# Performance work log

Measured on AMD Instinct MI355X. Metric: run time of the kernel, lower is better.

## Reference

```python
import jax, jax.numpy as jnp
import numpy as np

B, D, K = 8192, 128, 256
RHO = 1.0


def setup_inputs() -> dict:
    key = jax.random.key(0)
    k1, k2, k3 = jax.random.split(key, 3)
    h = jax.random.normal(k1, (B, D), dtype=jnp.float32)
    y = jax.random.randint(k2, (B,), 0, K, dtype=jnp.int64)
    centers = jax.random.normal(k3, (K, D), dtype=jnp.float32)  # nn.Parameter
    return {"h": h, "y": y, "centers": centers}


def reference(h, y, centers):
    # Pairwise squared distances h[b] vs centers[k]: (B, K)
    diff = h[:, None, :] - centers[None, :, :]          # (B, K, D) broadcast
    norm_sq = jnp.sum(diff * diff, axis=2)              # (B, K)
    # Gather distance to the true-class centroid
    distance = jnp.take_along_axis(norm_sq, y[:, None], axis=1)[:, 0]  # (B,)
    # logsumexp over negative euclidean distances
    logsum = jax.nn.logsumexp(-jnp.sqrt(norm_sq), axis=1)              # (B,)
    loss = jnp.mean(distance + logsum)                  # reduction='mean'
    # Regularization: repel nearest centroids (num_classes != 1)
    cdiff = centers[:, None, :] - centers[None, :, :]   # (K, K, D)
    pd = jnp.sum(cdiff * cdiff, axis=2)                 # squared cdist (K, K)
    pd = jnp.where(jnp.eye(K, dtype=bool), jnp.inf, pd)
    reg = jnp.sum(-jnp.min(jnp.log(pd), axis=-1))       # reduction='sum'
    return loss + RHO * reg
```

## Files before the change

kernel.cpp:

```cpp
#include <hip/hip_runtime.h>
#include <math.h>

typedef __attribute__((ext_vector_type(8))) __bf16 bf16x8;
typedef __attribute__((ext_vector_type(4))) float f32x4;

constexpr int B = 8192;
constexpr int D = 128;
constexpr int K = 256;
constexpr int MB = B / 16;


__global__ __launch_bounds__(256) void prep_kernel(const float* __restrict__ centers,
                                                   float* __restrict__ part_reg,
                                                   float* __restrict__ cc,
                                                   bf16x8* __restrict__ cbu) {
  __shared__ float red[4];
  const int lane = threadIdx.x & 63;
  const int wid  = threadIdx.x >> 6;
  if (blockIdx.x < K) {
    const int i = blockIdx.x;
    const int j = threadIdx.x;
    const float* ci = centers + (size_t)i * D;
    const float* cj = centers + (size_t)j * D;
    float pd = 0.f;
#pragma unroll
    for (int q = 0; q < D / 4; ++q) {
      float4 a  = reinterpret_cast<const float4*>(ci)[q];
      float4 bq = reinterpret_cast<const float4*>(cj)[q];
      float dx = a.x - bq.x, dy = a.y - bq.y, dz = a.z - bq.z, dw = a.w - bq.w;
      pd = fmaf(dx, dx, fmaf(dy, dy, fmaf(dz, dz, fmaf(dw, dw, pd))));
    }
    if (j == i) pd = INFINITY;
#pragma unroll
    for (int off = 32; off; off >>= 1) pd = fminf(pd, __shfl_xor(pd, off));
    if (lane == 0) red[wid] = pd;
    __syncthreads();
    if (threadIdx.x == 0) {
      float m = fminf(fminf(red[0], red[1]), fminf(red[2], red[3]));
      part_reg[i] = -logf(m);
    }
  } else {
    const int ci = blockIdx.x - K;
    const int t = threadIdx.x;
    const int base = ci * 2048 + t * 8;
    const float4* p = reinterpret_cast<const float4*>(centers + base);
    float4 f0 = p[0], f1 = p[1];
    bf16x8 o;
    o[0] = (__bf16)f0.x; o[1] = (__bf16)f0.y; o[2] = (__bf16)f0.z; o[3] = (__bf16)f0.w;
    o[4] = (__bf16)f1.x; o[5] = (__bf16)f1.y; o[6] = (__bf16)f1.z; o[7] = (__bf16)f1.w;
    cbu[ci * 256 + t] = o;
    float sq = f0.x * f0.x + f0.y * f0.y + f0.z * f0.z + f0.w * f0.w +
               f1.x * f1.x + f1.y * f1.y + f1.z * f1.z + f1.w * f1.w;
#pragma unroll
    for (int off = 1; off < 16; off <<= 1) sq += __shfl_xor(sq, off);
    if ((t & 15) == 0) cc[base / 128] = sq;
  }
}

__global__ __launch_bounds__(256) void main_kernel(
    const float* __restrict__ h, const int* __restrict__ y,
    const bf16x8* __restrict__ cbu, const float* __restrict__ cc,
    float* __restrict__ part_loss) {
  const int t = threadIdx.x;
  const int w = t >> 6;
  const int l = t & 63;
  const int lr = l & 15;
  const int lg = l >> 4;
  const int r0 = blockIdx.x * 16;
  const int n0 = w * 64;

  const float* hrow = h + (size_t)(r0 + lr) * D + lg * 8;
  bf16x8 a[4];
  float sq = 0.f;
#pragma unroll
  for (int c = 0; c < 4; ++c) {
    const float4* hp = reinterpret_cast<const float4*>(hrow + c * 32);
    float4 f0 = hp[0], f1 = hp[1];
    sq = fmaf(f0.x, f0.x, fmaf(f0.y, f0.y, fmaf(f0.z, f0.z, fmaf(f0.w, f0.w, sq))));
    sq = fmaf(f1.x, f1.x, fmaf(f1.y, f1.y, fmaf(f1.z, f1.z, fmaf(f1.w, f1.w, sq))));
    a[c][0] = (__bf16)f0.x; a[c][1] = (__bf16)f0.y;
    a[c][2] = (__bf16)f0.z; a[c][3] = (__bf16)f0.w;
    a[c][4] = (__bf16)f1.x; a[c][5] = (__bf16)f1.y;
    a[c][6] = (__bf16)f1.z; a[c][7] = (__bf16)f1.w;
  }
  sq += __shfl_xor(sq, 16);
  sq += __shfl_xor(sq, 32);
  float hh_r[4];
  int y_r[4];
#pragma unroll
  for (int j = 0; j < 4; ++j) {
    hh_r[j] = __int_as_float(
        __builtin_amdgcn_ds_bpermute((lg * 4 + j) << 2, __float_as_int(sq)));
    y_r[j] = y[r0 + lg * 4 + j];
  }

  f32x4 zero = {0.f, 0.f, 0.f, 0.f};
  f32x4 acc[4] = {zero, zero, zero, zero};
#pragma unroll
  for (int c = 0; c < 4; ++c) {
    bf16x8 bb[4];
#pragma unroll
    for (int n = 0; n < 4; ++n)
      bb[n] = cbu[(size_t)(n0 + n * 16 + lr) * (D / 8) + c * 4 + lg];
#pragma unroll
    for (int n = 0; n < 4; ++n)
      asm("v_mfma_f32_16x16x32_bf16 %0, %1, %2, %0"
          : "+v"(acc[n])
          : "v"(a[c]), "v"(bb[n]));
  }

  float s[4] = {0.f, 0.f, 0.f, 0.f};
  float dyv[4] = {0.f, 0.f, 0.f, 0.f};
#pragma unroll
  for (int n = 0; n < 4; ++n) {
    const int colg = n0 + n * 16 + lr;
    const float ccv = cc[colg];
#pragma unroll
    for (int j = 0; j < 4; ++j) {
      float dist = fmaxf(fmaf(-2.f, acc[n][j], hh_r[j] + ccv), 0.f);
      if (y_r[j] == colg) dyv[j] = dist;
      s[j] += __expf(-sqrtf(dist));
    }
  }
#pragma unroll
  for (int j = 0; j < 4; ++j) {
#pragma unroll
    for (int off = 1; off < 16; off <<= 1) {
      s[j] += __shfl_xor(s[j], off);
      dyv[j] += __shfl_xor(dyv[j], off);
    }
  }
  __shared__ float ls[4][16];
  __shared__ float ldy[4][16];
  if (lr == 0) {
#pragma unroll
    for (int j = 0; j < 4; ++j) {
      ls[w][lg * 4 + j] = s[j];
      ldy[w][lg * 4 + j] = dyv[j];
    }
  }
  __syncthreads();
  if (t < 16) {
    float stot = (ls[0][t] + ls[1][t]) + (ls[2][t] + ls[3][t]);
    float dtot = (ldy[0][t] + ldy[1][t]) + (ldy[2][t] + ldy[3][t]);
    float v = dtot + logf(stot);
#pragma unroll
    for (int off = 1; off < 16; off <<= 1) v += __shfl_xor(v, off);
    if (t == 0) part_loss[blockIdx.x] = v;
  }
}

__global__ __launch_bounds__(256) void final_kernel(
    const float* __restrict__ part_loss, const float* __restrict__ part_reg,
    float* __restrict__ out) {
  const int t = threadIdx.x;
  float v = part_reg[t] + (part_loss[t] + part_loss[t + 256]) * (1.0f / (float)B);
  const int lane = t & 63;
  const int wid  = t >> 6;
#pragma unroll
  for (int off = 32; off; off >>= 1) v += __shfl_xor(v, off);
  __shared__ float red[4];
  if (lane == 0) red[wid] = v;
  __syncthreads();
  if (t == 0) out[0] = red[0] + red[1] + red[2] + red[3];
}

extern "C" void kernel_launch(void* const* d_in, const int* in_sizes, int n_in,
                              void* d_out, int out_size, void* d_ws, size_t ws_size,
                              hipStream_t stream) {
  const float* h       = (const float*)d_in[0];
  const int*   y       = (const int*)d_in[1];
  const float* centers = (const float*)d_in[2];
  float* out = (float*)d_out;
  float* ws  = (float*)d_ws;

  float*  part_reg  = ws;
  float*  cc        = ws + 256;
  float*  part_loss = ws + 512;
  bf16x8* cbu       = reinterpret_cast<bf16x8*>(ws + 1024);

  prep_kernel<<<K + 16, 256, 0, stream>>>(centers, part_reg, cc, cbu);
  main_kernel<<<MB, 256, 0, stream>>>(h, y, cbu, cc, part_loss);
  final_kernel<<<1, 256, 0, stream>>>(part_loss, part_reg, out);
}
```

Baseline: 20.48 us.

## Fuse center prep into main kernel and compute reg via MFMA blocks

Removes the separate prep kernel. Each main-kernel block now converts fp32 centers to bf16 and computes their squared norms inline, and 16 extra blocks compute the centroid pairwise-min regularizer with the same MFMA path. This saves one kernel launch and the bf16/center-norm workspace round trip. In exchange every block redoes the center conversion, and the regularizer now uses a bf16 norm-expansion distance instead of exact fp32 differences, which risks precision loss in log(min pd).

```diff
diff --git a/kernel.cpp b/kernel.cpp
--- a/kernel.cpp
+++ b/kernel.cpp
@@ -1,160 +1,159 @@
 #include <hip/hip_runtime.h>
 #include <math.h>
 
-typedef __attribute__((ext_vector_type(8))) __bf16 bf16x8;
+typedef __attribute__((ext_vector_type(8))) short short8;
 typedef __attribute__((ext_vector_type(4))) float f32x4;
 
 constexpr int B = 8192;
 constexpr int D = 128;
 constexpr int K = 256;
-constexpr int MB = B / 16;
+constexpr int RB = K / 16;
+constexpr int HB = B / 16;
+constexpr int GRID = RB + HB;
 
 
-__global__ __launch_bounds__(256) void prep_kernel(const float* __restrict__ centers,
-                                                   float* __restrict__ part_reg,
-                                                   float* __restrict__ cc,
-                                                   bf16x8* __restrict__ cbu) {
-  __shared__ float red[4];
-  const int lane = threadIdx.x & 63;
-  const int wid  = threadIdx.x >> 6;
-  if (blockIdx.x < K) {
-    const int i = blockIdx.x;
-    const int j = threadIdx.x;
-    const float* ci = centers + (size_t)i * D;
-    const float* cj = centers + (size_t)j * D;
-    float pd = 0.f;
-#pragma unroll
-    for (int q = 0; q < D / 4; ++q) {
-      float4 a  = reinterpret_cast<const float4*>(ci)[q];
-      float4 bq = reinterpret_cast<const float4*>(cj)[q];
-      float dx = a.x - bq.x, dy = a.y - bq.y, dz = a.z - bq.z, dw = a.w - bq.w;
-      pd = fmaf(dx, dx, fmaf(dy, dy, fmaf(dz, dz, fmaf(dw, dw, pd))));
-    }
-    if (j == i) pd = INFINITY;
-#pragma unroll
-    for (int off = 32; off; off >>= 1) pd = fminf(pd, __shfl_xor(pd, off));
-    if (lane == 0) red[wid] = pd;
-    __syncthreads();
-    if (threadIdx.x == 0) {
-      float m = fminf(fminf(red[0], red[1]), fminf(red[2], red[3]));
-      part_reg[i] = -logf(m);
-    }
-  } else {
-    const int ci = blockIdx.x - K;
-    const int t = threadIdx.x;
-    const int base = ci * 2048 + t * 8;
-    const float4* p = reinterpret_cast<const float4*>(centers + base);
-    float4 f0 = p[0], f1 = p[1];
-    bf16x8 o;
-    o[0] = (__bf16)f0.x; o[1] = (__bf16)f0.y; o[2] = (__bf16)f0.z; o[3] = (__bf16)f0.w;
-    o[4] = (__bf16)f1.x; o[5] = (__bf16)f1.y; o[6] = (__bf16)f1.z; o[7] = (__bf16)f1.w;
-    cbu[ci * 256 + t] = o;
-    float sq = f0.x * f0.x + f0.y * f0.y + f0.z * f0.z + f0.w * f0.w +
-               f1.x * f1.x + f1.y * f1.y + f1.z * f1.z + f1.w * f1.w;
-#pragma unroll
-    for (int off = 1; off < 16; off <<= 1) sq += __shfl_xor(sq, off);
-    if ((t & 15) == 0) cc[base / 128] = sq;
-  }
+__device__ __forceinline__ short8 cvt8(float4 f0, float4 f1, float& sq) {
+  sq = fmaf(f0.x, f0.x, fmaf(f0.y, f0.y, fmaf(f0.z, f0.z, fmaf(f0.w, f0.w, sq))));
+  sq = fmaf(f1.x, f1.x, fmaf(f1.y, f1.y, fmaf(f1.z, f1.z, fmaf(f1.w, f1.w, sq))));
+  union { short8 s; __bf16 b[8]; } u;
+  u.b[0] = (__bf16)f0.x; u.b[1] = (__bf16)f0.y;
+  u.b[2] = (__bf16)f0.z; u.b[3] = (__bf16)f0.w;
+  u.b[4] = (__bf16)f1.x; u.b[5] = (__bf16)f1.y;
+  u.b[6] = (__bf16)f1.z; u.b[7] = (__bf16)f1.w;
+  return u.s;
 }
 
 __global__ __launch_bounds__(256) void main_kernel(
     const float* __restrict__ h, const int* __restrict__ y,
-    const bf16x8* __restrict__ cbu, const float* __restrict__ cc,
-    float* __restrict__ part_loss) {
+    const float* __restrict__ centers,
+    float* __restrict__ part_loss, float* __restrict__ part_reg_sum) {
   const int t = threadIdx.x;
   const int w = t >> 6;
   const int l = t & 63;
   const int lr = l & 15;
   const int lg = l >> 4;
-  const int r0 = blockIdx.x * 16;
+  const bool isreg = (blockIdx.x < RB);
+  const int r0 = (isreg ? (int)blockIdx.x : (int)blockIdx.x - RB) * 16;
+  const float* Ap = (isreg ? centers : h) + (size_t)(r0 + lr) * D + lg * 8;
   const int n0 = w * 64;
 
-  const float* hrow = h + (size_t)(r0 + lr) * D + lg * 8;
-  bf16x8 a[4];
+  short8 a[4];
   float sq = 0.f;
 #pragma unroll
   for (int c = 0; c < 4; ++c) {
-    const float4* hp = reinterpret_cast<const float4*>(hrow + c * 32);
-    float4 f0 = hp[0], f1 = hp[1];
-    sq = fmaf(f0.x, f0.x, fmaf(f0.y, f0.y, fmaf(f0.z, f0.z, fmaf(f0.w, f0.w, sq))));
-    sq = fmaf(f1.x, f1.x, fmaf(f1.y, f1.y, fmaf(f1.z, f1.z, fmaf(f1.w, f1.w, sq))));
-    a[c][0] = (__bf16)f0.x; a[c][1] = (__bf16)f0.y;
-    a[c][2] = (__bf16)f0.z; a[c][3] = (__bf16)f0.w;
-    a[c][4] = (__bf16)f1.x; a[c][5] = (__bf16)f1.y;
-    a[c][6] = (__bf16)f1.z; a[c][7] = (__bf16)f1.w;
+    const float4* p = reinterpret_cast<const float4*>(Ap + c * 32);
+    a[c] = cvt8(p[0], p[1], sq);
   }
   sq += __shfl_xor(sq, 16);
   sq += __shfl_xor(sq, 32);
-  float hh_r[4];
-  int y_r[4];
+  float rr[4];
 #pragma unroll
-  for (int j = 0; j < 4; ++j) {
-    hh_r[j] = __int_as_float(
+  for (int j = 0; j < 4; ++j)
+    rr[j] = __int_as_float(
         __builtin_amdgcn_ds_bpermute((lg * 4 + j) << 2, __float_as_int(sq)));
-    y_r[j] = y[r0 + lg * 4 + j];
-  }
 
   f32x4 zero = {0.f, 0.f, 0.f, 0.f};
   f32x4 acc[4] = {zero, zero, zero, zero};
+  float cs[4] = {0.f, 0.f, 0.f, 0.f};
 #pragma unroll
   for (int c = 0; c < 4; ++c) {
-    bf16x8 bb[4];
 #pragma unroll
-    for (int n = 0; n < 4; ++n)
-      bb[n] = cbu[(size_t)(n0 + n * 16 + lr) * (D / 8) + c * 4 + lg];
-#pragma unroll
-    for (int n = 0; n < 4; ++n)
-      asm("v_mfma_f32_16x16x32_bf16 %0, %1, %2, %0"
-          : "+v"(acc[n])
-          : "v"(a[c]), "v"(bb[n]));
-  }
-
-  float s[4] = {0.f, 0.f, 0.f, 0.f};
-  float dyv[4] = {0.f, 0.f, 0.f, 0.f};
-#pragma unroll
-  for (int n = 0; n < 4; ++n) {
-    const int colg = n0 + n * 16 + lr;
-    const float ccv = cc[colg];
-#pragma unroll
-    for (int j = 0; j < 4; ++j) {
-      float dist = fmaxf(fmaf(-2.f, acc[n][j], hh_r[j] + ccv), 0.f);
-      if (y_r[j] == colg) dyv[j] = dist;
-      s[j] += __expf(-sqrtf(dist));
+    for (int n = 0; n < 4; ++n) {
+      const float4* p = reinterpret_cast<const float4*>(
+          centers + (size_t)(n0 + n * 16 + lr) * D + c * 32 + lg * 8);
+      short8 bfrag = cvt8(p[0], p[1], cs[n]);
+      acc[n] = __builtin_amdgcn_mfma_f32_16x16x32_bf16(a[c], bfrag, acc[n], 0, 0, 0);
     }
   }
 #pragma unroll
-  for (int j = 0; j < 4; ++j) {
-#pragma unroll
-    for (int off = 1; off < 16; off <<= 1) {
-      s[j] += __shfl_xor(s[j], off);
-      dyv[j] += __shfl_xor(dyv[j], off);
-    }
+  for (int n = 0; n < 4; ++n) {
+    cs[n] += __shfl_xor(cs[n], 16);
+    cs[n] += __shfl_xor(cs[n], 32);
   }
+
   __shared__ float ls[4][16];
   __shared__ float ldy[4][16];
-  if (lr == 0) {
+
+  if (!isreg) {
+    int y_r[4];
+#pragma unroll
+    for (int j = 0; j < 4; ++j) y_r[j] = y[r0 + lg * 4 + j];
+    float s[4] = {0.f, 0.f, 0.f, 0.f}, dyv[4] = {0.f, 0.f, 0.f, 0.f};
+#pragma unroll
+    for (int n = 0; n < 4; ++n) {
+      const int colg = n0 + n * 16 + lr;
+      const float ccv = cs[n];
+#pragma unroll
+      for (int j = 0; j < 4; ++j) {
+        float dist = fmaxf(fmaf(-2.f, acc[n][j], rr[j] + ccv), 0.f);
+        if (y_r[j] == colg) dyv[j] = dist;
+        s[j] += __expf(-sqrtf(dist));
+      }
+    }
 #pragma unroll
     for (int j = 0; j < 4; ++j) {
-      ls[w][lg * 4 + j] = s[j];
-      ldy[w][lg * 4 + j] = dyv[j];
+#pragma unroll
+      for (int off = 1; off < 16; off <<= 1) {
+        s[j]   += __shfl_xor(s[j], off);
+        dyv[j] += __shfl_xor(dyv[j], off);
+      }
     }
-  }
-  __syncthreads();
-  if (t < 16) {
-    float stot = (ls[0][t] + ls[1][t]) + (ls[2][t] + ls[3][t]);
-    float dtot = (ldy[0][t] + ldy[1][t]) + (ldy[2][t] + ldy[3][t]);
-    float v = dtot + logf(stot);
+    if (lr == 0) {
 #pragma unroll
-    for (int off = 1; off < 16; off <<= 1) v += __shfl_xor(v, off);
-    if (t == 0) part_loss[blockIdx.x] = v;
+      for (int j = 0; j < 4; ++j) {
+        ls[w][lg * 4 + j]  = s[j];
+        ldy[w][lg * 4 + j] = dyv[j];
+      }
+    }
+    __syncthreads();
+    if (t < 16) {
+      float stot = (ls[0][t] + ls[1][t]) + (ls[2][t] + ls[3][t]);
+      float dtot = (ldy[0][t] + ldy[1][t]) + (ldy[2][t] + ldy[3][t]);
+      float v = dtot + logf(fmaxf(stot, 1e-37f));
+#pragma unroll
+      for (int off = 1; off < 16; off <<= 1) v += __shfl_xor(v, off);
+      if (t == 0) part_loss[blockIdx.x - RB] = v;
+    }
+  } else {
+    float pmin[4] = {INFINITY, INFINITY, INFINITY, INFINITY};
+#pragma unroll
+    for (int n = 0; n < 4; ++n) {
+      const int colg = n0 + n * 16 + lr;
+      const float ccv = cs[n];
+#pragma unroll
+      for (int j = 0; j < 4; ++j) {
+        const int irow = r0 + lg * 4 + j;
+        float pd = fmaf(-2.f, acc[n][j], rr[j] + ccv);
+        if (colg != irow) pmin[j] = fminf(pmin[j], pd);
+      }
+    }
+#pragma unroll
+    for (int j = 0; j < 4; ++j) {
+#pragma unroll
+      for (int off = 1; off < 16; off <<= 1)
+        pmin[j] = fminf(pmin[j], __shfl_xor(pmin[j], off));
+    }
+    if (lr == 0) {
+#pragma unroll
+      for (int j = 0; j < 4; ++j) ls[w][lg * 4 + j] = pmin[j];
+    }
+    __syncthreads();
+    if (t < 16) {
+      float m = fminf(fminf(ls[0][t], ls[1][t]), fminf(ls[2][t], ls[3][t]));
+      float v = -logf(fmaxf(m, 1e-37f));
+#pragma unroll
+      for (int off = 1; off < 16; off <<= 1) v += __shfl_xor(v, off);
+      if (t == 0) part_reg_sum[blockIdx.x] = v;
+    }
   }
 }
 
 __global__ __launch_bounds__(256) void final_kernel(
-    const float* __restrict__ part_loss, const float* __restrict__ part_reg,
+    const float* __restrict__ part_loss, const float* __restrict__ part_reg_sum,
     float* __restrict__ out) {
   const int t = threadIdx.x;
-  float v = part_reg[t] + (part_loss[t] + part_loss[t + 256]) * (1.0f / (float)B);
+  float v = (part_loss[t] + part_loss[t + 256]) * (1.0f / (float)B);
+  if (t < RB) v += part_reg_sum[t];
   const int lane = t & 63;
   const int wid  = t >> 6;
 #pragma unroll
@@ -174,12 +173,9 @@
   float* out = (float*)d_out;
   float* ws  = (float*)d_ws;
 
-  float*  part_reg  = ws;
-  float*  cc        = ws + 256;
-  float*  part_loss = ws + 512;
-  bf16x8* cbu       = reinterpret_cast<bf16x8*>(ws + 1024);
+  float* part_loss    = ws;
+  float* part_reg_sum = ws + 512;
 
-  prep_kernel<<<K + 16, 256, 0, stream>>>(centers, part_reg, cc, cbu);
-  main_kernel<<<MB, 256, 0, stream>>>(h, y, cbu, cc, part_loss);
-  final_kernel<<<1, 256, 0, stream>>>(part_loss, part_reg, out);
+  main_kernel<<<GRID, 256, 0, stream>>>(h, y, centers, part_loss, part_reg_sum);
+  final_kernel<<<1, 256, 0, stream>>>(part_loss, part_reg_sum, out);
 }
```

Measured after the change: 22.27 us. +8.7%, slower.
